# Kernel optimization log

Hardware: AMD Instinct MI355X
Metric: run time of the kernel (lower is better)

The kernel has to match this reference:

```python
import jax, jax.numpy as jnp
import numpy as np

INF = 3000.0  # 'inf' constant from the source module


def setup_inputs() -> dict:
    key = jax.random.key(0)
    k1, k2, k3 = jax.random.split(key, 3)
    B, n_RoI, H = 32, 512, 768
    encI = jax.random.normal(k1, (B, n_RoI, H), dtype=jnp.float32)
    RoI_mask = jax.random.randint(k2, (B, n_RoI), 0, 2).astype(jnp.int32)
    spatials = jax.random.uniform(k3, (B, n_RoI, 6), dtype=jnp.float32)
    return {"encI": encI, "RoI_mask": RoI_mask, "spatials": spatials, "k": 5}


def _gen_nearest_mask(spatials, RoI_mask, k, eye):
    # centers of boxes; padded boxes are pushed far away (center + INF)
    cx = (spatials[..., 0] + spatials[..., 2]) * 0.5
    cy = (spatials[..., 1] + spatials[..., 3]) * 0.5
    center = jnp.stack([cx, cy], axis=-1)                      # (B, n, 2)
    center = jnp.where(RoI_mask.astype(bool)[..., None], center, center + INF)
    diff = center[:, :, None, :] - center[:, None, :, :]       # (B, n, n, 2)
    dist = jnp.linalg.norm(diff, axis=-1)                      # (B, n, n)
    # self-distance set to INF*INF so self is never among k nearest
    dist = dist * (1.0 - eye) + eye * (INF * INF)
    _, idx = jax.lax.top_k(-dist, k)                           # k smallest -> (B, n, k)
    B, n = dist.shape[0], dist.shape[1]
    b_ix = jnp.arange(B)[:, None, None]
    r_ix = jnp.arange(n)[None, :, None]
    topk_mask = jnp.zeros_like(dist).at[b_ix, r_ix, idx].set(1.0)
    topk_mask = topk_mask * (1.0 - eye)                        # zero self-mask
    topk_mask = topk_mask * RoI_mask.astype(dist.dtype)[:, None, :]  # zero padded columns
    return topk_mask


def reference(encI, RoI_mask, spatials, k):
    B, n, H = encI.shape
    eye = jnp.eye(n, dtype=encI.dtype)
    # dot-product similarity, diagonal zeroed
    sim = jnp.einsum('bih,bjh->bij', encI, encI) * (1.0 - eye)
    topk_mask = _gen_nearest_mask(spatials, RoI_mask, k, eye)
    # keep similarity only at topk neighbors, zeros elsewhere;
    # softmax is over the FULL row (zeros included), faithful to the source
    w = jnp.where(topk_mask > 0, sim, jnp.zeros_like(sim))
    w = jax.nn.softmax(w, axis=-1)                             # (B, n, n)
    neighbor_context = jnp.einsum('bij,bjh->bih', w, encI)     # (B, n, H)
    return jnp.concatenate([encI, neighbor_context], axis=-1)  # (B, n, 2H)
```

## Files before the change

### kernel.cpp

```cpp
#include <hip/hip_runtime.h>
#include <cfloat>
#include <cstddef>

#define NB 32
#define NN 512
#define NH 768
#define H4 (NH / 4)
#define ROWS (NB * NN)
#define MAXK 8
#define CHUNKS 32
#define RPC (NN / CHUNKS)
#define INF_C 3000.0f
#define SELF_D 9000000.0f

typedef float f32x4 __attribute__((ext_vector_type(4)));

__device__ __forceinline__ void nt_store4(float4* p, float4 v) {
  f32x4 t; t.x = v.x; t.y = v.y; t.z = v.z; t.w = v.w;
  __builtin_nontemporal_store(t, (f32x4*)p);
}

template <int CTRL>
__device__ __forceinline__ int dpp_i(int x) {
  return __builtin_amdgcn_update_dpp(0, x, CTRL, 0xF, 0xF, true);
}
template <int CTRL>
__device__ __forceinline__ float dpp_f(float x) {
  return __int_as_float(dpp_i<CTRL>(__float_as_int(x)));
}

__device__ __forceinline__ float wave_sum64(float x) {
  x += dpp_f<0xB1>(x);
  x += dpp_f<0x4E>(x);
  x += dpp_f<0x141>(x);
  x += dpp_f<0x140>(x);
  int xi = __float_as_int(x);
  float a = __int_as_float(__builtin_amdgcn_readlane(xi, 0));
  float b = __int_as_float(__builtin_amdgcn_readlane(xi, 16));
  float c = __int_as_float(__builtin_amdgcn_readlane(xi, 32));
  float d = __int_as_float(__builtin_amdgcn_readlane(xi, 48));
  return (a + b) + (c + d);
}

#define ARGMIN_COMBINE(ov, oj)                                       \
  do {                                                               \
    float _ov = (ov); int _oj = (oj);                                \
    if (_ov < bv || (_ov == bv && _oj < bj)) { bv = _ov; bj = _oj; } \
  } while (0)

__global__ __launch_bounds__(256) void prep_kernel(const float* __restrict__ sp,
                                                   const int* __restrict__ mask,
                                                   const float4* __restrict__ e4,
                                                   float2* __restrict__ ctr,
                                                   float4* __restrict__ part) {
  int bid = blockIdx.x;
  if (bid < 768) {
    int t = bid * 256 + threadIdx.x;
    int h4 = t % H4;
    int bc = t / H4;
    int b = bc >> 5, chunk = bc & 31;
    const float4* p = e4 + ((size_t)(b * NN + chunk * RPC)) * H4 + h4;
    float ax = 0.f, ay = 0.f, az = 0.f, aw = 0.f;
#pragma unroll
    for (int r = 0; r < RPC; ++r) {
      float4 v = p[(size_t)r * H4];
      ax += v.x; ay += v.y; az += v.z; aw += v.w;
    }
    part[t] = make_float4(ax, ay, az, aw);
  } else {
    int t = (bid - 768) * 256 + threadIdx.x;
    const float* s = sp + (size_t)t * 6;
    float cx = __fmul_rn(__fadd_rn(s[0], s[2]), 0.5f);
    float cy = __fmul_rn(__fadd_rn(s[1], s[3]), 0.5f);
    if (mask[t] == 0) { cx = __fadd_rn(cx, INF_C); cy = __fadd_rn(cy, INF_C); }
    ctr[t] = make_float2(cx, cy);
  }
}

__global__ __launch_bounds__(256) void rowsum_reduce_kernel(const float4* __restrict__ part,
                                                            float4* __restrict__ S4) {
  int t = blockIdx.x * 256 + threadIdx.x;
  int h4 = t % H4;
  int b = t / H4;
  float ax = 0.f, ay = 0.f, az = 0.f, aw = 0.f;
#pragma unroll
  for (int c = 0; c < CHUNKS; ++c) {
    float4 v = part[(size_t)(b * CHUNKS + c) * H4 + h4];
    ax += v.x; ay += v.y; az += v.z; aw += v.w;
  }
  S4[t] = make_float4(ax, ay, az, aw);
}

template <int K, bool GUARD>
__device__ __forceinline__ void fuse_body(const float2* __restrict__ ctr,
                                          const int* __restrict__ mask,
                                          const float4* __restrict__ S4,
                                          const float4* __restrict__ e4,
                                          float4* __restrict__ out4,
                                          int row, int b, int i, int lane, int k) {
  const float4* erow = e4 + (size_t)row * H4;
  float4 ei[3];
#pragma unroll
  for (int q = 0; q < 3; ++q) ei[q] = erow[q * 64 + lane];
  float4 Sv[3];
#pragma unroll
  for (int q = 0; q < 3; ++q) Sv[q] = S4[b * H4 + q * 64 + lane];

  float2 ci = ctr[b * NN + i];
  float dv[8];
#pragma unroll
  for (int c = 0; c < 8; ++c) {
    int j = c * 64 + lane;
    float2 cj = ctr[b * NN + j];
    float dx = __fadd_rn(ci.x, -cj.x);
    float dy = __fadd_rn(ci.y, -cj.y);
    float d = __fsqrt_rn(__fadd_rn(__fmul_rn(dx, dx), __fmul_rn(dy, dy)));
    dv[c] = (j == i) ? SELF_D : d;
  }

  int sel[K];
  int valid[K];
  float4 ej[K][3];
#pragma unroll
  for (int s = 0; s < K; ++s) {
    sel[s] = 0;
    valid[s] = 0;
    if (!GUARD || s < k) {
      float bv = FLT_MAX;
      int bj = 1 << 30;
#pragma unroll
      for (int c = 0; c < 8; ++c) {
        int j = c * 64 + lane;
        if (dv[c] < bv) { bv = dv[c]; bj = j; }
      }
      ARGMIN_COMBINE(dpp_f<0xB1>(bv), dpp_i<0xB1>(bj));
      ARGMIN_COMBINE(dpp_f<0x4E>(bv), dpp_i<0x4E>(bj));
      ARGMIN_COMBINE(dpp_f<0x141>(bv), dpp_i<0x141>(bj));
      ARGMIN_COMBINE(dpp_f<0x140>(bv), dpp_i<0x140>(bj));
      int bvi = __float_as_int(bv);
      unsigned long long k0 =
          ((unsigned long long)(unsigned)__builtin_amdgcn_readlane(bvi, 0) << 32) |
          (unsigned)__builtin_amdgcn_readlane(bj, 0);
      unsigned long long k1 =
          ((unsigned long long)(unsigned)__builtin_amdgcn_readlane(bvi, 16) << 32) |
          (unsigned)__builtin_amdgcn_readlane(bj, 16);
      unsigned long long k2 =
          ((unsigned long long)(unsigned)__builtin_amdgcn_readlane(bvi, 32) << 32) |
          (unsigned)__builtin_amdgcn_readlane(bj, 32);
      unsigned long long k3 =
          ((unsigned long long)(unsigned)__builtin_amdgcn_readlane(bvi, 48) << 32) |
          (unsigned)__builtin_amdgcn_readlane(bj, 48);
      unsigned long long kb = k0 < k1 ? k0 : k1;
      unsigned long long kc = k2 < k3 ? k2 : k3;
      kb = kb < kc ? kb : kc;
      int js = (int)(unsigned)kb;
      sel[s] = js;
#pragma unroll
      for (int c = 0; c < 8; ++c)
        if (c * 64 + lane == js) dv[c] = FLT_MAX;
      const float4* ero = e4 + (size_t)(b * NN + js) * H4;
#pragma unroll
      for (int q = 0; q < 3; ++q) ej[s][q] = ero[q * 64 + lane];
      valid[s] = mask[b * NN + js];
    }
  }

  float d[K];
#pragma unroll
  for (int s = 0; s < K; ++s) {
    float p = 0.f;
#pragma unroll
    for (int q = 0; q < 3; ++q) {
      p = fmaf(ei[q].x, ej[s][q].x, p);
      p = fmaf(ei[q].y, ej[s][q].y, p);
      p = fmaf(ei[q].z, ej[s][q].z, p);
      p = fmaf(ei[q].w, ej[s][q].w, p);
    }
    d[s] = wave_sum64(p);
  }

  float M = 0.f;
  int m = 0;
#pragma unroll
  for (int s = 0; s < K; ++s)
    if (valid[s]) { ++m; M = fmaxf(M, d[s]); }
  float e0 = expf(-M);
  float Z = (float)(NN - m) * e0;
  float es[K];
#pragma unroll
  for (int s = 0; s < K; ++s) {
    es[s] = valid[s] ? expf(d[s] - M) : 0.f;
    Z += es[s];
  }
  float invZ = 1.0f / Z;
  float c0 = e0 * invZ;

  float4 ctx[3];
#pragma unroll
  for (int q = 0; q < 3; ++q) {
    ctx[q].x = c0 * Sv[q].x; ctx[q].y = c0 * Sv[q].y;
    ctx[q].z = c0 * Sv[q].z; ctx[q].w = c0 * Sv[q].w;
  }
#pragma unroll
  for (int s = 0; s < K; ++s) {
    if (valid[s]) {
      float cs = es[s] * invZ - c0;
#pragma unroll
      for (int q = 0; q < 3; ++q) {
        ctx[q].x = fmaf(cs, ej[s][q].x, ctx[q].x);
        ctx[q].y = fmaf(cs, ej[s][q].y, ctx[q].y);
        ctx[q].z = fmaf(cs, ej[s][q].z, ctx[q].z);
        ctx[q].w = fmaf(cs, ej[s][q].w, ctx[q].w);
      }
    }
  }

  size_t ob = (size_t)row * (2 * H4);
#pragma unroll
  for (int q = 0; q < 3; ++q) nt_store4(out4 + ob + q * 64 + lane, ei[q]);
#pragma unroll
  for (int q = 0; q < 3; ++q) nt_store4(out4 + ob + H4 + q * 64 + lane, ctx[q]);
}

__global__ __launch_bounds__(256) void fuse_kernel(const float2* __restrict__ ctr,
                                                   const float4* __restrict__ e4,
                                                   const int* __restrict__ mask,
                                                   const float4* __restrict__ S4,
                                                   const int* __restrict__ kptr,
                                                   float4* __restrict__ out4) {
  int bid = blockIdx.x;
  int swz = (bid & 7) * (ROWS / 4 / 8) + (bid >> 3);
  int wid = threadIdx.x >> 6;
  int lane = threadIdx.x & 63;
  int row = swz * 4 + wid;
  int b = row >> 9;
  int i = row & (NN - 1);
  int k = *kptr;
  if (k == 5) {
    fuse_body<5, false>(ctr, mask, S4, e4, out4, row, b, i, lane, 5);
  } else {
    if (k > MAXK) k = MAXK;
    if (k < 0) k = 0;
    fuse_body<MAXK, true>(ctr, mask, S4, e4, out4, row, b, i, lane, k);
  }
}

extern "C" void kernel_launch(void* const* d_in, const int* in_sizes, int n_in,
                              void* d_out, int out_size, void* d_ws, size_t ws_size,
                              hipStream_t stream) {
  const float* encI = (const float*)d_in[0];
  const int* RoI_mask = (const int*)d_in[1];
  const float* spatials = (const float*)d_in[2];
  const int* kptr = (const int*)d_in[3];

  const size_t ctr_bytes = (size_t)ROWS * sizeof(float2);
  const size_t s4_bytes = (size_t)NB * H4 * sizeof(float4);
  const size_t part_bytes = (size_t)NB * CHUNKS * H4 * sizeof(float4);

  float2* ctr = (float2*)d_ws;
  float4* S4 = (float4*)((char*)d_ws + ctr_bytes);
  float4* part;
  if (ws_size >= ctr_bytes + s4_bytes + part_bytes) {
    part = (float4*)((char*)d_ws + ctr_bytes + s4_bytes);
  } else {
    part = (float4*)d_out;
  }

  prep_kernel<<<832, 256, 0, stream>>>(spatials, RoI_mask, (const float4*)encI, ctr, part);
  rowsum_reduce_kernel<<<24, 256, 0, stream>>>(part, S4);
  fuse_kernel<<<ROWS / 4, 256, 0, stream>>>(ctr, (const float4*)encI, RoI_mask, S4, kptr,
                                            (float4*)d_out);
  (void)in_sizes; (void)n_in; (void)out_size;
}
```

Before: 47.19 us.

## Stream neighbor rows with online softmax to cut register pressure

Neighbor selection now only records indices. Each selected neighbor's embedding slice is then loaded, dotted with the row, and folded into a running online-softmax accumulator, so the kernel no longer holds K×3 float4 neighbor buffers in registers. The S4 column-sum load is moved to the epilogue, and launch bounds request 8 waves per SIMD to raise occupancy. In exchange, each neighbor now costs extra exp calls and a serial dependency, and the embedding loads are no longer issued all at once during selection, which reduces memory-level parallelism.

```diff
diff --git a/kernel.cpp b/kernel.cpp
--- a/kernel.cpp
+++ b/kernel.cpp
@@ -102,9 +102,6 @@
   float4 ei[3];
 #pragma unroll
   for (int q = 0; q < 3; ++q) ei[q] = erow[q * 64 + lane];
-  float4 Sv[3];
-#pragma unroll
-  for (int q = 0; q < 3; ++q) Sv[q] = S4[b * H4 + q * 64 + lane];
 
   float2 ci = ctr[b * NN + i];
   float dv[8];
@@ -119,12 +116,9 @@
   }
 
   int sel[K];
-  int valid[K];
-  float4 ej[K][3];
 #pragma unroll
   for (int s = 0; s < K; ++s) {
     sel[s] = 0;
-    valid[s] = 0;
     if (!GUARD || s < k) {
       float bv = FLT_MAX;
       int bj = 1 << 30;
@@ -158,76 +152,80 @@
 #pragma unroll
       for (int c = 0; c < 8; ++c)
         if (c * 64 + lane == js) dv[c] = FLT_MAX;
+    }
+  }
+
+  float M = 0.f, e0 = 1.f, sumE = 0.f;
+  int m = 0;
+  float4 ctxA[3];
+#pragma unroll
+  for (int q = 0; q < 3; ++q) ctxA[q] = make_float4(0.f, 0.f, 0.f, 0.f);
+
+#pragma unroll
+  for (int s = 0; s < K; ++s) {
+    if (!GUARD || s < k) {
+      int js = sel[s];
+      int vld = mask[b * NN + js];
       const float4* ero = e4 + (size_t)(b * NN + js) * H4;
-#pragma unroll
-      for (int q = 0; q < 3; ++q) ej[s][q] = ero[q * 64 + lane];
-      valid[s] = mask[b * NN + js];
-    }
-  }
-
-  float d[K];
-#pragma unroll
-  for (int s = 0; s < K; ++s) {
-    float p = 0.f;
-#pragma unroll
-    for (int q = 0; q < 3; ++q) {
-      p = fmaf(ei[q].x, ej[s][q].x, p);
-      p = fmaf(ei[q].y, ej[s][q].y, p);
-      p = fmaf(ei[q].z, ej[s][q].z, p);
-      p = fmaf(ei[q].w, ej[s][q].w, p);
-    }
-    d[s] = wave_sum64(p);
-  }
-
-  float M = 0.f;
-  int m = 0;
-#pragma unroll
-  for (int s = 0; s < K; ++s)
-    if (valid[s]) { ++m; M = fmaxf(M, d[s]); }
-  float e0 = expf(-M);
-  float Z = (float)(NN - m) * e0;
-  float es[K];
-#pragma unroll
-  for (int s = 0; s < K; ++s) {
-    es[s] = valid[s] ? expf(d[s] - M) : 0.f;
-    Z += es[s];
-  }
-  float invZ = 1.0f / Z;
-  float c0 = e0 * invZ;
-
-  float4 ctx[3];
-#pragma unroll
-  for (int q = 0; q < 3; ++q) {
-    ctx[q].x = c0 * Sv[q].x; ctx[q].y = c0 * Sv[q].y;
-    ctx[q].z = c0 * Sv[q].z; ctx[q].w = c0 * Sv[q].w;
-  }
-#pragma unroll
-  for (int s = 0; s < K; ++s) {
-    if (valid[s]) {
-      float cs = es[s] * invZ - c0;
-#pragma unroll
-      for (int q = 0; q < 3; ++q) {
-        ctx[q].x = fmaf(cs, ej[s][q].x, ctx[q].x);
-        ctx[q].y = fmaf(cs, ej[s][q].y, ctx[q].y);
-        ctx[q].z = fmaf(cs, ej[s][q].z, ctx[q].z);
-        ctx[q].w = fmaf(cs, ej[s][q].w, ctx[q].w);
+      float4 ej0 = ero[0 * 64 + lane];
+      float4 ej1 = ero[1 * 64 + lane];
+      float4 ej2 = ero[2 * 64 + lane];
+      float p = 0.f;
+      p = fmaf(ei[0].x, ej0.x, p); p = fmaf(ei[0].y, ej0.y, p);
+      p = fmaf(ei[0].z, ej0.z, p); p = fmaf(ei[0].w, ej0.w, p);
+      p = fmaf(ei[1].x, ej1.x, p); p = fmaf(ei[1].y, ej1.y, p);
+      p = fmaf(ei[1].z, ej1.z, p); p = fmaf(ei[1].w, ej1.w, p);
+      p = fmaf(ei[2].x, ej2.x, p); p = fmaf(ei[2].y, ej2.y, p);
+      p = fmaf(ei[2].z, ej2.z, p); p = fmaf(ei[2].w, ej2.w, p);
+      float ds = wave_sum64(p);
+      if (vld) {
+        ++m;
+        float nm = fmaxf(M, ds);
+        float scale = expf(M - nm);
+        float es = expf(ds - nm);
+        M = nm;
+        e0 = expf(-nm);
+        sumE = fmaf(sumE, scale, es);
+        float w = es - e0;
+        ctxA[0].x = fmaf(ctxA[0].x, scale, w * ej0.x);
+        ctxA[0].y = fmaf(ctxA[0].y, scale, w * ej0.y);
+        ctxA[0].z = fmaf(ctxA[0].z, scale, w * ej0.z);
+        ctxA[0].w = fmaf(ctxA[0].w, scale, w * ej0.w);
+        ctxA[1].x = fmaf(ctxA[1].x, scale, w * ej1.x);
+        ctxA[1].y = fmaf(ctxA[1].y, scale, w * ej1.y);
+        ctxA[1].z = fmaf(ctxA[1].z, scale, w * ej1.z);
+        ctxA[1].w = fmaf(ctxA[1].w, scale, w * ej1.w);
+        ctxA[2].x = fmaf(ctxA[2].x, scale, w * ej2.x);
+        ctxA[2].y = fmaf(ctxA[2].y, scale, w * ej2.y);
+        ctxA[2].z = fmaf(ctxA[2].z, scale, w * ej2.z);
+        ctxA[2].w = fmaf(ctxA[2].w, scale, w * ej2.w);
       }
     }
   }
 
+  float Z = fmaf((float)(NN - m), e0, sumE);
+  float invZ = 1.0f / Z;
   size_t ob = (size_t)row * (2 * H4);
 #pragma unroll
   for (int q = 0; q < 3; ++q) nt_store4(out4 + ob + q * 64 + lane, ei[q]);
 #pragma unroll
-  for (int q = 0; q < 3; ++q) nt_store4(out4 + ob + H4 + q * 64 + lane, ctx[q]);
-}
-
-__global__ __launch_bounds__(256) void fuse_kernel(const float2* __restrict__ ctr,
-                                                   const float4* __restrict__ e4,
-                                                   const int* __restrict__ mask,
-                                                   const float4* __restrict__ S4,
-                                                   const int* __restrict__ kptr,
-                                                   float4* __restrict__ out4) {
+  for (int q = 0; q < 3; ++q) {
+    float4 Sv = S4[b * H4 + q * 64 + lane];
+    float4 cx;
+    cx.x = invZ * fmaf(e0, Sv.x, ctxA[q].x);
+    cx.y = invZ * fmaf(e0, Sv.y, ctxA[q].y);
+    cx.z = invZ * fmaf(e0, Sv.z, ctxA[q].z);
+    cx.w = invZ * fmaf(e0, Sv.w, ctxA[q].w);
+    nt_store4(out4 + ob + H4 + q * 64 + lane, cx);
+  }
+}
+
+__global__ __launch_bounds__(256, 8) void fuse_kernel(const float2* __restrict__ ctr,
+                                                      const float4* __restrict__ e4,
+                                                      const int* __restrict__ mask,
+                                                      const float4* __restrict__ S4,
+                                                      const int* __restrict__ kptr,
+                                                      float4* __restrict__ out4) {
   int bid = blockIdx.x;
   int swz = (bid & 7) * (ROWS / 4 / 8) + (bid >> 3);
   int wid = threadIdx.x >> 6;
```

After: 44.64 us. -5.4%, faster.

## Cut register pressure in fuse kernel by re-reading neighbor rows per chunk

Applied to the files above, without the earlier changes.

Neighbor rows are no longer held in registers across the whole selection phase. They are loaded chunk by chunk for the dot products and loaded again for the context accumulation, with the S vector loaded late and the self copy of the row stored early. Launch bounds now request 8 blocks per multiprocessor, which lowers the register budget. The aim is higher occupancy to hide memory latency, at the cost of reading the neighbor rows twice (likely from cache) and serialising the gather after the top-k search.

```diff
diff --git a/kernel.cpp b/kernel.cpp
--- a/kernel.cpp
+++ b/kernel.cpp
@@ -102,9 +102,6 @@
   float4 ei[3];
 #pragma unroll
   for (int q = 0; q < 3; ++q) ei[q] = erow[q * 64 + lane];
-  float4 Sv[3];
-#pragma unroll
-  for (int q = 0; q < 3; ++q) Sv[q] = S4[b * H4 + q * 64 + lane];
 
   float2 ci = ctr[b * NN + i];
   float dv[8];
@@ -119,12 +116,9 @@
   }
 
   int sel[K];
-  int valid[K];
-  float4 ej[K][3];
 #pragma unroll
   for (int s = 0; s < K; ++s) {
     sel[s] = 0;
-    valid[s] = 0;
     if (!GUARD || s < k) {
       float bv = FLT_MAX;
       int bj = 1 << 30;
@@ -158,26 +152,41 @@
 #pragma unroll
       for (int c = 0; c < 8; ++c)
         if (c * 64 + lane == js) dv[c] = FLT_MAX;
-      const float4* ero = e4 + (size_t)(b * NN + js) * H4;
-#pragma unroll
-      for (int q = 0; q < 3; ++q) ej[s][q] = ero[q * 64 + lane];
-      valid[s] = mask[b * NN + js];
-    }
-  }
-
+    }
+  }
+
+  size_t ob = (size_t)row * (2 * H4);
+#pragma unroll
+  for (int q = 0; q < 3; ++q) nt_store4(out4 + ob + q * 64 + lane, ei[q]);
+
+  int valid[K];
+#pragma unroll
+  for (int s = 0; s < K; ++s)
+    valid[s] = (!GUARD || s < k) ? mask[b * NN + sel[s]] : 0;
+
+  float p[K];
+#pragma unroll
+  for (int s = 0; s < K; ++s) p[s] = 0.f;
+#pragma unroll
+  for (int q = 0; q < 3; ++q) {
+    float4 t[K];
+#pragma unroll
+    for (int s = 0; s < K; ++s)
+      if (!GUARD || s < k)
+        t[s] = e4[(size_t)(b * NN + sel[s]) * H4 + q * 64 + lane];
+#pragma unroll
+    for (int s = 0; s < K; ++s) {
+      if (!GUARD || s < k) {
+        p[s] = fmaf(ei[q].x, t[s].x, p[s]);
+        p[s] = fmaf(ei[q].y, t[s].y, p[s]);
+        p[s] = fmaf(ei[q].z, t[s].z, p[s]);
+        p[s] = fmaf(ei[q].w, t[s].w, p[s]);
+      }
+    }
+  }
   float d[K];
 #pragma unroll
-  for (int s = 0; s < K; ++s) {
-    float p = 0.f;
-#pragma unroll
-    for (int q = 0; q < 3; ++q) {
-      p = fmaf(ei[q].x, ej[s][q].x, p);
-      p = fmaf(ei[q].y, ej[s][q].y, p);
-      p = fmaf(ei[q].z, ej[s][q].z, p);
-      p = fmaf(ei[q].w, ej[s][q].w, p);
-    }
-    d[s] = wave_sum64(p);
-  }
+  for (int s = 0; s < K; ++s) d[s] = (!GUARD || s < k) ? wave_sum64(p[s]) : 0.f;
 
   float M = 0.f;
   int m = 0;
@@ -194,40 +203,45 @@
   }
   float invZ = 1.0f / Z;
   float c0 = e0 * invZ;
+  float cs[K];
+#pragma unroll
+  for (int s = 0; s < K; ++s) cs[s] = valid[s] ? (es[s] * invZ - c0) : 0.f;
 
   float4 ctx[3];
 #pragma unroll
   for (int q = 0; q < 3; ++q) {
-    ctx[q].x = c0 * Sv[q].x; ctx[q].y = c0 * Sv[q].y;
-    ctx[q].z = c0 * Sv[q].z; ctx[q].w = c0 * Sv[q].w;
-  }
-#pragma unroll
-  for (int s = 0; s < K; ++s) {
-    if (valid[s]) {
-      float cs = es[s] * invZ - c0;
-#pragma unroll
-      for (int q = 0; q < 3; ++q) {
-        ctx[q].x = fmaf(cs, ej[s][q].x, ctx[q].x);
-        ctx[q].y = fmaf(cs, ej[s][q].y, ctx[q].y);
-        ctx[q].z = fmaf(cs, ej[s][q].z, ctx[q].z);
-        ctx[q].w = fmaf(cs, ej[s][q].w, ctx[q].w);
+    float4 Sv = S4[b * H4 + q * 64 + lane];
+    ctx[q].x = c0 * Sv.x; ctx[q].y = c0 * Sv.y;
+    ctx[q].z = c0 * Sv.z; ctx[q].w = c0 * Sv.w;
+  }
+#pragma unroll
+  for (int q = 0; q < 3; ++q) {
+    float4 t[K];
+#pragma unroll
+    for (int s = 0; s < K; ++s)
+      if (valid[s])
+        t[s] = e4[(size_t)(b * NN + sel[s]) * H4 + q * 64 + lane];
+#pragma unroll
+    for (int s = 0; s < K; ++s) {
+      if (valid[s]) {
+        ctx[q].x = fmaf(cs[s], t[s].x, ctx[q].x);
+        ctx[q].y = fmaf(cs[s], t[s].y, ctx[q].y);
+        ctx[q].z = fmaf(cs[s], t[s].z, ctx[q].z);
+        ctx[q].w = fmaf(cs[s], t[s].w, ctx[q].w);
       }
     }
   }
 
-  size_t ob = (size_t)row * (2 * H4);
-#pragma unroll
-  for (int q = 0; q < 3; ++q) nt_store4(out4 + ob + q * 64 + lane, ei[q]);
 #pragma unroll
   for (int q = 0; q < 3; ++q) nt_store4(out4 + ob + H4 + q * 64 + lane, ctx[q]);
 }
 
-__global__ __launch_bounds__(256) void fuse_kernel(const float2* __restrict__ ctr,
-                                                   const float4* __restrict__ e4,
-                                                   const int* __restrict__ mask,
-                                                   const float4* __restrict__ S4,
-                                                   const int* __restrict__ kptr,
-                                                   float4* __restrict__ out4) {
+__global__ __launch_bounds__(256, 8) void fuse_kernel(const float2* __restrict__ ctr,
+                                                      const float4* __restrict__ e4,
+                                                      const int* __restrict__ mask,
+                                                      const float4* __restrict__ S4,
+                                                      const int* __restrict__ kptr,
+                                                      float4* __restrict__ out4) {
   int bid = blockIdx.x;
   int swz = (bid & 7) * (ROWS / 4 / 8) + (bid >> 3);
   int wid = threadIdx.x >> 6;
```

After: 117.0 us. 148% more time.
